# Kernel tuning notes

Measured on AMD Instinct MI355X. Metric: run time of the kernel, lower is better.

## Reference

```python
import jax, jax.numpy as jnp
import numpy as np

D_MODEL, N_HEADS, D_FF = 1024, 16, 4096
B, L, PREFIX = 2, 2048, 512
EPS = 1e-5


def _ln(x, w, b):
    mu = jnp.mean(x, axis=-1, keepdims=True)
    var = jnp.mean((x - mu) ** 2, axis=-1, keepdims=True)
    return (x - mu) * jax.lax.rsqrt(var + EPS) * w + b


def setup_inputs() -> dict:
    key = jax.random.key(0)
    ks = jax.random.split(key, 5)
    d, f = D_MODEL, D_FF
    return {
        "x": jax.random.normal(ks[0], (B, L, d), jnp.float32),
        "ln1_w": jnp.ones((d,), jnp.float32),
        "ln1_b": jnp.zeros((d,), jnp.float32),
        "in_proj_w": jax.random.normal(ks[1], (3 * d, d), jnp.float32) / np.sqrt(d),
        "in_proj_b": jnp.zeros((3 * d,), jnp.float32),
        "out_w": jax.random.normal(ks[2], (d, d), jnp.float32) / np.sqrt(d),
        "out_b": jnp.zeros((d,), jnp.float32),
        "ln2_w": jnp.ones((d,), jnp.float32),
        "ln2_b": jnp.zeros((d,), jnp.float32),
        "fc1_w": jax.random.normal(ks[3], (f, d), jnp.float32) / np.sqrt(d),
        "fc1_b": jnp.zeros((f,), jnp.float32),
        "fc2_w": jax.random.normal(ks[4], (d, f), jnp.float32) / np.sqrt(f),
        "fc2_b": jnp.zeros((d,), jnp.float32),
        "prefix_len": PREFIX,
    }


def reference(x, ln1_w, ln1_b, in_proj_w, in_proj_b, out_w, out_b,
              ln2_w, ln2_b, fc1_w, fc1_b, fc2_w, fc2_b, prefix_len):
    Bv, Lv, d = x.shape
    H = N_HEADS
    hd = d // H
    m = prefix_len

    # additive prefix-decoder mask (L, L): allowed if j < m, or (i >= m and j <= i)
    i = jnp.arange(Lv)[:, None]
    j = jnp.arange(Lv)[None, :]
    allowed = (j < m) | ((i >= m) & (j <= i))
    mask = jnp.where(allowed, 0.0, -jnp.inf).astype(x.dtype)

    h = _ln(x, ln1_w, ln1_b)
    qkv = h @ in_proj_w.T + in_proj_b                      # [B, L, 3d]
    q, k, v = jnp.split(qkv, 3, axis=-1)
    q = q.reshape(Bv, Lv, H, hd)
    k = k.reshape(Bv, Lv, H, hd)
    v = v.reshape(Bv, Lv, H, hd)
    scale = 1.0 / np.sqrt(hd)
    scores = jnp.einsum("bihd,bjhd->bhij", q, k) * scale   # [B, H, L, L]
    attn = jax.nn.softmax(scores + mask, axis=-1)
    ctx = jnp.einsum("bhij,bjhd->bihd", attn, v).reshape(Bv, Lv, d)
    sa = ctx @ out_w.T + out_b
    x = x + sa

    h = _ln(x, ln2_w, ln2_b)
    ff = jax.nn.gelu(h @ fc1_w.T + fc1_b, approximate=False) @ fc2_w.T + fc2_b
    return x + ff
```

## Files before the change

kernel.cpp:

```cpp
#include <hip/hip_runtime.h>
#include <cstdint>
#include <cstddef>

#define DM   1024
#define NH   16
#define HD   64
#define DFF  4096
#define BB   2
#define LL   2048
#define MM   (BB*LL)

using short8 = __attribute__((ext_vector_type(8))) short;
using f32x4  = __attribute__((ext_vector_type(4))) float;

__device__ __forceinline__ unsigned short f2bf(float f) {
  union { float f; uint32_t u; } v; v.f = f;
  uint32_t u = v.u;
  uint32_t r = (u + 0x7fffu + ((u >> 16) & 1u)) >> 16;
  return (unsigned short)r;
}

__device__ __forceinline__ uint32_t cvtpk_bf16(float a, float b) {
  uint32_t r;
  asm("v_cvt_pk_bf16_f32 %0, %1, %2" : "=v"(r) : "v"(a), "v"(b));
  return r;
}

__device__ __forceinline__ float exp2_fast(float x) {
  float r;
  asm("v_exp_f32 %0, %1" : "=v"(r) : "v"(x));
  return r;
}

__device__ __forceinline__ float rcp_fast(float x) {
  float r;
  asm("v_rcp_f32 %0, %1" : "=v"(r) : "v"(x));
  return r;
}

__device__ __forceinline__ float gelu_tanh(float v) {
  float y = v * (0.7978845608028654f + 0.035677408136300125f * v * v);
  float e = exp2_fast(y * 2.885390081777927f);
  float tnh = 1.0f - 2.0f * rcp_fast(1.0f + e);
  return 0.5f * v * (1.0f + tnh);
}

#define GLDS16(gp, lp) \
  __builtin_amdgcn_global_load_lds((const __attribute__((address_space(1))) uint32_t*)(gp), \
                                   (__attribute__((address_space(3))) uint32_t*)(lp), 16, 0, 0)

__device__ __forceinline__ void ln_row_body(const float* __restrict__ x,
                                            const float* __restrict__ w,
                                            const float* __restrict__ b,
                                            unsigned short* __restrict__ out,
                                            int row, int t) {
  float4 v = ((const float4*)(x + (size_t)row * DM))[t];
  float s  = v.x + v.y + v.z + v.w;
  float sq = v.x*v.x + v.y*v.y + v.z*v.z + v.w*v.w;
  #pragma unroll
  for (int o = 32; o; o >>= 1) { s += __shfl_down(s, o); sq += __shfl_down(sq, o); }
  __shared__ float sh[8];
  if ((t & 63) == 0) { sh[t >> 6] = s; sh[4 + (t >> 6)] = sq; }
  __syncthreads();
  float S  = sh[0] + sh[1] + sh[2] + sh[3];
  float SQ = sh[4] + sh[5] + sh[6] + sh[7];
  float mu  = S * (1.0f / DM);
  float var = SQ * (1.0f / DM) - mu * mu;
  float rs  = rsqrtf(var + 1e-5f);
  float4 wv = ((const float4*)w)[t];
  float4 bv = ((const float4*)b)[t];
  ushort4 o;
  o.x = f2bf((v.x - mu) * rs * wv.x + bv.x);
  o.y = f2bf((v.y - mu) * rs * wv.y + bv.y);
  o.z = f2bf((v.z - mu) * rs * wv.z + bv.z);
  o.w = f2bf((v.w - mu) * rs * wv.w + bv.w);
  ((ushort4*)(out + (size_t)row * DM))[t] = o;
}

__global__ __launch_bounds__(256) void convert_f32_bf16(const float* __restrict__ in,
                                                        unsigned short* __restrict__ out, int n4) {
  int i = blockIdx.x * 256 + threadIdx.x;
  if (i < n4) {
    float4 v = ((const float4*)in)[i];
    ushort4 o;
    o.x = f2bf(v.x); o.y = f2bf(v.y); o.z = f2bf(v.z); o.w = f2bf(v.w);
    ((ushort4*)out)[i] = o;
  }
}

__global__ __launch_bounds__(256) void prep_kernel(const float* __restrict__ x,
                                                   const float* __restrict__ ln1_w,
                                                   const float* __restrict__ ln1_b,
                                                   unsigned short* __restrict__ h1,
                                                   const float* __restrict__ s0, unsigned short* __restrict__ d0, int n0,
                                                   const float* __restrict__ s1, unsigned short* __restrict__ d1, int n1,
                                                   const float* __restrict__ s2, unsigned short* __restrict__ d2, int n2,
                                                   const float* __restrict__ s3, unsigned short* __restrict__ d3, int n3) {
  if (blockIdx.x < MM) {
    ln_row_body(x, ln1_w, ln1_b, h1, blockIdx.x, threadIdx.x);
    return;
  }
  const int cb = blockIdx.x - MM;
  const int tid = cb * 256 + threadIdx.x;
  const int stride = (gridDim.x - MM) * 256;
  for (int i = tid; i < n0; i += stride) {
    float4 v = ((const float4*)s0)[i];
    ushort4 o; o.x = f2bf(v.x); o.y = f2bf(v.y); o.z = f2bf(v.z); o.w = f2bf(v.w);
    ((ushort4*)d0)[i] = o;
  }
  for (int i = tid; i < n1; i += stride) {
    float4 v = ((const float4*)s1)[i];
    ushort4 o; o.x = f2bf(v.x); o.y = f2bf(v.y); o.z = f2bf(v.z); o.w = f2bf(v.w);
    ((ushort4*)d1)[i] = o;
  }
  for (int i = tid; i < n2; i += stride) {
    float4 v = ((const float4*)s2)[i];
    ushort4 o; o.x = f2bf(v.x); o.y = f2bf(v.y); o.z = f2bf(v.z); o.w = f2bf(v.w);
    ((ushort4*)d2)[i] = o;
  }
  for (int i = tid; i < n3; i += stride) {
    float4 v = ((const float4*)s3)[i];
    ushort4 o; o.x = f2bf(v.x); o.y = f2bf(v.y); o.z = f2bf(v.z); o.w = f2bf(v.w);
    ((ushort4*)d3)[i] = o;
  }
}

__global__ __launch_bounds__(256) void ln_kernel(const float* __restrict__ x,
                                                 const float* __restrict__ w,
                                                 const float* __restrict__ b,
                                                 unsigned short* __restrict__ out) {
  ln_row_body(x, w, b, out, blockIdx.x, threadIdx.x);
}

template <int EPI, int VT>
__global__ __launch_bounds__(512) void gemm8(const unsigned short* __restrict__ A,
                                             const unsigned short* __restrict__ Bw,
                                             const float* __restrict__ bias,
                                             unsigned short* __restrict__ Cout,
                                             unsigned short* __restrict__ vt,
                                             int M, int N, int K, int lda, int ldb) {
  __shared__ unsigned short As[2][256 * 64];
  __shared__ unsigned short Bs[2][256 * 64];
  const int t = threadIdx.x;
  const int l = t & 63, lr = l & 15, lg = l >> 4;
  const int wid = t >> 6, wm = wid >> 2, wn = wid & 3;

  int bx = blockIdx.x, by = blockIdx.y;
  {
    const int gx = gridDim.x;
    const int total = gx * gridDim.y;
    if ((total & 7) == 0) {
      int lin = by * gx + bx;
      int lin2 = (lin & 7) * (total >> 3) + (lin >> 3);
      bx = lin2 % gx;
      by = lin2 / gx;
    }
  }
  const int m0 = by * 256, n0 = bx * 256;

  f32x4 acc[8][4];
  #pragma unroll
  for (int mi = 0; mi < 8; ++mi)
    #pragma unroll
    for (int ni = 0; ni < 4; ++ni) acc[mi][ni] = {0.f, 0.f, 0.f, 0.f};

  const int rowt = t >> 3, sw = (t & 7) ^ (rowt & 7);
  const unsigned short* Ag = A  + (size_t)(m0 + rowt) * lda + sw * 8;
  const unsigned short* Bg = Bw + (size_t)(n0 + rowt) * ldb + sw * 8;
  const size_t r64A = (size_t)64 * lda;
  const size_t r64B = (size_t)64 * ldb;

  const int rs = lr & 7;
  const int segA = (lg ^ rs) * 8;
  const int segB = ((lg + 4) ^ rs) * 8;

  const int nt = K >> 6;

  auto stage = [&](int kt, int buf) {
    const int k0 = kt << 6;
    char* Ad = (char*)&As[buf][0] + t * 16;
    char* Bd = (char*)&Bs[buf][0] + t * 16;
    #pragma unroll
    for (int g = 0; g < 4; ++g) GLDS16(Ag + k0 + g * r64A, Ad + g * 8192);
    #pragma unroll
    for (int g = 0; g < 4; ++g) GLDS16(Bg + k0 + g * r64B, Bd + g * 8192);
  };

  auto compute = [&](const unsigned short* __restrict__ Ab,
                     const unsigned short* __restrict__ Bb) {
    short8 bfr[4][2];
    #pragma unroll
    for (int ni = 0; ni < 4; ++ni) {
      const int row = wn * 64 + ni * 16 + lr;
      bfr[ni][0] = *(const short8*)&Bb[row * 64 + segA];
      bfr[ni][1] = *(const short8*)&Bb[row * 64 + segB];
    }
    __builtin_amdgcn_s_setprio(1);
    #pragma unroll
    for (int mp = 0; mp < 4; ++mp) {
      short8 af[2][2];
      #pragma unroll
      for (int q = 0; q < 2; ++q) {
        const int row = wm * 128 + (mp * 2 + q) * 16 + lr;
        af[q][0] = *(const short8*)&Ab[row * 64 + segA];
        af[q][1] = *(const short8*)&Ab[row * 64 + segB];
      }
      #pragma unroll
      for (int q = 0; q < 2; ++q)
        #pragma unroll
        for (int ni = 0; ni < 4; ++ni) {
          acc[mp * 2 + q][ni] = __builtin_amdgcn_mfma_f32_16x16x32_bf16(af[q][0], bfr[ni][0], acc[mp * 2 + q][ni], 0, 0, 0);
          acc[mp * 2 + q][ni] = __builtin_amdgcn_mfma_f32_16x16x32_bf16(af[q][1], bfr[ni][1], acc[mp * 2 + q][ni], 0, 0, 0);
        }
    }
    __builtin_amdgcn_s_setprio(0);
  };

  stage(0, 0);
  __syncthreads();

  for (int kt = 0; kt < nt; kt += 2) {
    if (kt + 1 < nt) stage(kt + 1, 1);
    compute(As[0], Bs[0]);
    __syncthreads();
    if (kt + 2 < nt) stage(kt + 2, 0);
    compute(As[1], Bs[1]);
    __syncthreads();
  }

  if (VT && n0 >= 2 * DM) {
    #pragma unroll
    for (int mi = 0; mi < 8; ++mi) {
      int row = m0 + wm * 128 + mi * 16 + lg * 4;
      int b = row >> 11, j = row & (LL - 1);
      #pragma unroll
      for (int ni = 0; ni < 4; ++ni) {
        int col = n0 + wn * 64 + ni * 16 + lr;
        int hd_ = col - 2 * DM;
        float bv = bias[col];
        uint2 pk;
        pk.x = cvtpk_bf16(acc[mi][ni][0] + bv, acc[mi][ni][1] + bv);
        pk.y = cvtpk_bf16(acc[mi][ni][2] + bv, acc[mi][ni][3] + bv);
        *(uint2*)&vt[(size_t)(b * 1024 + hd_) * LL + j] = pk;
      }
    }
    return;
  }

  #pragma unroll
  for (int mi = 0; mi < 8; ++mi) {
    int row = m0 + wm * 128 + mi * 16 + lg * 4;
    #pragma unroll
    for (int ni = 0; ni < 4; ++ni) {
      int col = n0 + wn * 64 + ni * 16 + lr;
      float bv = bias[col];
      #pragma unroll
      for (int r = 0; r < 4; ++r) {
        float v = acc[mi][ni][r] + bv;
        size_t idx = (size_t)(row + r) * N + col;
        if (EPI == 0) {
          Cout[idx] = f2bf(v);
        } else {
          Cout[idx] = f2bf(gelu_tanh(v));
        }
      }
    }
  }
}

template <int EPI, int BM>
__global__ __launch_bounds__(256) void gemm_bt(const unsigned short* __restrict__ A,
                                               const unsigned short* __restrict__ Bw,
                                               const float* __restrict__ bias,
                                               const float* __restrict__ res,
                                               void* __restrict__ Cout,
                                               int M, int N, int K, int lda, int ldb) {
  constexpr int MI   = BM / 32;
  constexpr int ABUF = BM * 64;
  __shared__ unsigned short As[2 * ABUF];
  __shared__ unsigned short Bs[2 * 64 * 64];
  const int t = threadIdx.x;
  const int l = t & 63, lr = l & 15, lg = l >> 4;
  const int w = t >> 6, wm = w >> 1, wn = w & 1;

  int bx = blockIdx.x, by = blockIdx.y;
  {
    const int gx = gridDim.x;
    const int total = gx * gridDim.y;
    if ((total & 7) == 0) {
      int lin = by * gx + bx;
      int lin2 = (lin & 7) * (total >> 3) + (lin >> 3);
      bx = lin2 % gx;
      by = lin2 / gx;
    }
  }
  const int m0 = by * BM, n0 = bx * 64;

  f32x4 acc[MI][2];
  #pragma unroll
  for (int mi = 0; mi < MI; ++mi)
    #pragma unroll
    for (int ni = 0; ni < 2; ++ni) acc[mi][ni] = {0.f, 0.f, 0.f, 0.f};

  const int rowt = t >> 3, sw = (t & 7) ^ (rowt & 7);
  const unsigned short* Ag = A  + (size_t)(m0 + rowt) * lda + sw * 8;
  const unsigned short* Bg = Bw + (size_t)(n0 + rowt) * ldb + sw * 8;
  char* AsB = (char*)As + t * 16;
  char* BsB = (char*)Bs + t * 16;
  const size_t r32A = (size_t)32 * lda;
  const size_t r32B = (size_t)32 * ldb;

  const int rs = lr & 7;
  const int segA = (lg ^ rs) * 8;
  const int segB = ((lg + 4) ^ rs) * 8;

  #pragma unroll
  for (int g = 0; g < MI; ++g) GLDS16(Ag + g * r32A, AsB + g * 4096);
  GLDS16(Bg,        BsB);
  GLDS16(Bg + r32B, BsB + 4096);

  int cur = 0;
  for (int k0 = 0; k0 < K; k0 += 64, cur ^= 1) {
    __syncthreads();
    const int kn = k0 + 64;
    if (kn < K) {
      char* An = AsB + (cur ^ 1) * (ABUF * 2);
      char* Bn = BsB + (cur ^ 1) * 8192;
      #pragma unroll
      for (int g = 0; g < MI; ++g) GLDS16(Ag + kn + g * r32A, An + g * 4096);
      GLDS16(Bg + kn,        Bn);
      GLDS16(Bg + kn + r32B, Bn + 4096);
    }
    const unsigned short* Ab = As + cur * ABUF;
    const unsigned short* Bb = Bs + cur * (64 * 64);
    short8 af[MI][2], bfr[2][2];
    #pragma unroll
    for (int mi = 0; mi < MI; ++mi) {
      const int row = wm * (BM / 2) + mi * 16 + lr;
      af[mi][0] = *(const short8*)&Ab[row * 64 + segA];
      af[mi][1] = *(const short8*)&Ab[row * 64 + segB];
    }
    #pragma unroll
    for (int ni = 0; ni < 2; ++ni) {
      const int row = wn * 32 + ni * 16 + lr;
      bfr[ni][0] = *(const short8*)&Bb[row * 64 + segA];
      bfr[ni][1] = *(const short8*)&Bb[row * 64 + segB];
    }
    #pragma unroll
    for (int mi = 0; mi < MI; ++mi)
      #pragma unroll
      for (int ni = 0; ni < 2; ++ni) {
        acc[mi][ni] = __builtin_amdgcn_mfma_f32_16x16x32_bf16(af[mi][0], bfr[ni][0], acc[mi][ni], 0, 0, 0);
        acc[mi][ni] = __builtin_amdgcn_mfma_f32_16x16x32_bf16(af[mi][1], bfr[ni][1], acc[mi][ni], 0, 0, 0);
      }
  }

  #pragma unroll
  for (int mi = 0; mi < MI; ++mi) {
    int row = m0 + wm * (BM / 2) + mi * 16 + lg * 4;
    #pragma unroll
    for (int ni = 0; ni < 2; ++ni) {
      int col = n0 + wn * 32 + ni * 16 + lr;
      float bv = (EPI == 3) ? 0.f : bias[col];
      #pragma unroll
      for (int r = 0; r < 4; ++r) {
        float v = acc[mi][ni][r] + bv;
        size_t idx = (size_t)(row + r) * N + col;
        if (EPI == 0) {
          ((unsigned short*)Cout)[idx] = f2bf(v);
        } else if (EPI == 1) {
          ((float*)Cout)[idx] = res[idx] + v;
        } else if (EPI == 2) {
          ((unsigned short*)Cout)[idx] = f2bf(gelu_tanh(v));
        } else {
          ((float*)Cout)[idx] += v;
        }
      }
    }
  }
}

__global__ __launch_bounds__(512) void attn_kernel(const unsigned short* __restrict__ qkv,
                                                   const unsigned short* __restrict__ vt,
                                                   const int* __restrict__ prefix,
                                                   unsigned short* __restrict__ ctx) {
  __shared__ unsigned short Ks[2][64 * 64];
  __shared__ unsigned short Vs[2][64 * 64];
  __shared__ unsigned short Plds[8][16][72];
  const int t = threadIdx.x, w = t >> 6, l = t & 63, lr = l & 15, lg = l >> 4;
  const int bh = blockIdx.y, b = bh >> 4, h = bh & 15;
  const int ib = gridDim.x - 1 - blockIdx.x;
  const int i0 = ib * 128, iw = i0 + w * 16;
  const int m = *prefix;
  const float C = 0.125f * 1.44269504088896f;

  const int r0 = t >> 3, s0 = t & 7, swz = s0 ^ (r0 & 7);
  const unsigned short* Kg0 = qkv + (size_t)(b * LL + r0) * 3072 + DM + h * 64 + swz * 8;
  const unsigned short* Vg0 = vt + (size_t)(bh * 64 + r0) * LL + swz * 8;
  char* KdB = (char*)Ks + t * 16;
  char* VdB = (char*)Vs + t * 16;
  const int rs = lr & 7;
  const int segA = (lg ^ rs) * 8;
  const int segB = ((lg + 4) ^ rs) * 8;

  short8 qf[2];
  {
    const unsigned short* qrow = qkv + (size_t)(b * LL + iw + lr) * 3072 + h * 64;
    qf[0] = *(const short8*)(qrow + lg * 8);
    qf[1] = *(const short8*)(qrow + 32 + lg * 8);
  }
  short8 ones;
  #pragma unroll
  for (int e = 0; e < 8; ++e) ones[e] = (short)0x3F80;

  f32x4 Ot[4];
  #pragma unroll
  for (int dt = 0; dt < 4; ++dt) Ot[dt] = {0.f, 0.f, 0.f, 0.f};
  f32x4 Osum = {0.f, 0.f, 0.f, 0.f};

  const int jmax = (i0 + 128 <= m) ? m : (i0 + 128);
  const int nb = (jmax + 63) >> 6;
  const int i_abs = iw + lr;

  GLDS16(Kg0, KdB);
  GLDS16(Vg0, VdB);

  for (int c = 0; c < nb; ++c) {
    __syncthreads();
    if (c + 1 < nb) {
      const size_t jn = (size_t)(c + 1) * 64;
      const int pn = (c + 1) & 1;
      GLDS16(Kg0 + jn * 3072, KdB + pn * 8192);
      GLDS16(Vg0 + jn,        VdB + pn * 8192);
    }
    const int jt = c * 64, p = c & 1;

    f32x4 sc[4];
    #pragma unroll
    for (int nt = 0; nt < 4; ++nt) {
      sc[nt] = {0.f, 0.f, 0.f, 0.f};
      const int row = nt * 16 + lr;
      short8 kf0 = *(const short8*)&Ks[p][row * 64 + segA];
      short8 kf1 = *(const short8*)&Ks[p][row * 64 + segB];
      sc[nt] = __builtin_amdgcn_mfma_f32_16x16x32_bf16(kf0, qf[0], sc[nt], 0, 0, 0);
      sc[nt] = __builtin_amdgcn_mfma_f32_16x16x32_bf16(kf1, qf[1], sc[nt], 0, 0, 0);
    }
    const bool full = (jt + 64 <= m) || (iw >= m && jt + 64 <= iw + 1);
    #pragma unroll
    for (int nt = 0; nt < 4; ++nt) {
      float p0 = exp2_fast(sc[nt][0] * C);
      float p1 = exp2_fast(sc[nt][1] * C);
      float p2 = exp2_fast(sc[nt][2] * C);
      float p3 = exp2_fast(sc[nt][3] * C);
      if (!full) {
        const int jb = jt + nt * 16 + lg * 4;
        const bool causal_i = (i_abs >= m);
        p0 = ((jb + 0 < m) || (causal_i && jb + 0 <= i_abs)) ? p0 : 0.f;
        p1 = ((jb + 1 < m) || (causal_i && jb + 1 <= i_abs)) ? p1 : 0.f;
        p2 = ((jb + 2 < m) || (causal_i && jb + 2 <= i_abs)) ? p2 : 0.f;
        p3 = ((jb + 3 < m) || (causal_i && jb + 3 <= i_abs)) ? p3 : 0.f;
      }
      uint2 pk;
      pk.x = cvtpk_bf16(p0, p1);
      pk.y = cvtpk_bf16(p2, p3);
      *(uint2*)&Plds[w][lr][nt * 16 + lg * 4] = pk;
    }
    short8 paf0 = *(const short8*)&Plds[w][lr][lg * 8];
    short8 paf1 = *(const short8*)&Plds[w][lr][32 + lg * 8];
    #pragma unroll
    for (int dt = 0; dt < 4; ++dt) {
      const int row = dt * 16 + lr;
      short8 vf0 = *(const short8*)&Vs[p][row * 64 + segA];
      short8 vf1 = *(const short8*)&Vs[p][row * 64 + segB];
      Ot[dt] = __builtin_amdgcn_mfma_f32_16x16x32_bf16(paf0, vf0, Ot[dt], 0, 0, 0);
      Ot[dt] = __builtin_amdgcn_mfma_f32_16x16x32_bf16(paf1, vf1, Ot[dt], 0, 0, 0);
    }
    Osum = __builtin_amdgcn_mfma_f32_16x16x32_bf16(paf0, ones, Osum, 0, 0, 0);
    Osum = __builtin_amdgcn_mfma_f32_16x16x32_bf16(paf1, ones, Osum, 0, 0, 0);
  }
  #pragma unroll
  for (int r = 0; r < 4; ++r) {
    float inv = 1.0f / Osum[r];
    size_t row = (size_t)(b * LL + iw + lg * 4 + r);
    #pragma unroll
    for (int dt = 0; dt < 4; ++dt)
      ctx[row * DM + h * 64 + dt * 16 + lr] = f2bf(Ot[dt][r] * inv);
  }
}

extern "C" void kernel_launch(void* const* d_in, const int* in_sizes, int n_in,
                              void* d_out, int out_size, void* d_ws, size_t ws_size,
                              hipStream_t stream) {
  const float* x        = (const float*)d_in[0];
  const float* ln1_w    = (const float*)d_in[1];
  const float* ln1_b    = (const float*)d_in[2];
  const float* in_proj_w= (const float*)d_in[3];
  const float* in_proj_b= (const float*)d_in[4];
  const float* out_w    = (const float*)d_in[5];
  const float* out_b    = (const float*)d_in[6];
  const float* ln2_w    = (const float*)d_in[7];
  const float* ln2_b    = (const float*)d_in[8];
  const float* fc1_w    = (const float*)d_in[9];
  const float* fc1_b    = (const float*)d_in[10];
  const float* fc2_w    = (const float*)d_in[11];
  const float* fc2_b    = (const float*)d_in[12];
  const int*   prefix   = (const int*)d_in[13];
  float* outp = (float*)d_out;

  char* ws = (char*)d_ws;
  unsigned short* slab  = (unsigned short*)ws;
  float*          x2    = (float*)(ws + ((size_t)8 << 20));
  unsigned short* vtb   = (unsigned short*)(ws + ((size_t)8 << 20));
  unsigned short* wslab = (unsigned short*)(ws + ((size_t)24 << 20));
  unsigned short* qkv   = (unsigned short*)(ws + ((size_t)32 << 20));
  unsigned short* wfc2  = (unsigned short*)(ws + ((size_t)32 << 20));
  unsigned short* ffh   = (unsigned short*)(ws + ((size_t)40 << 20));
  const bool big = ws_size >= ((size_t)72 << 20);
  const bool wd  = ws_size >= ((size_t)80 << 20);

  unsigned short* w_in  = (unsigned short*)(ws + ((size_t)24 << 20));
  unsigned short* w_out = (unsigned short*)(ws + ((size_t)30 << 20));
  unsigned short* w_fc1 = (unsigned short*)(ws + ((size_t)64 << 20));
  unsigned short* w_fc2 = (unsigned short*)(ws + ((size_t)72 << 20));
  unsigned short* ffm32 = (unsigned short*)(ws + ((size_t)32 << 20));

  if (wd) {
    prep_kernel<<<MM + 1024, 256, 0, stream>>>(x, ln1_w, ln1_b, slab,
                                               in_proj_w, w_in, 3072 * 1024 / 4,
                                               out_w, w_out, 1024 * 1024 / 4,
                                               fc1_w, w_fc1, 4096 * 1024 / 4,
                                               fc2_w, w_fc2, 1024 * 4096 / 4);
  } else {
    convert_f32_bf16<<<3072, 256, 0, stream>>>(in_proj_w, wslab, 3072 * 1024 / 4);
    ln_kernel<<<MM, 256, 0, stream>>>(x, ln1_w, ln1_b, slab);
  }

  gemm8<0, 1><<<dim3(3072 / 256, MM / 256), 512, 0, stream>>>(slab, wd ? w_in : wslab, in_proj_b, qkv, vtb, MM, 3072, 1024, 1024, 1024);
  attn_kernel<<<dim3(LL / 128, BB * NH), 512, 0, stream>>>(qkv, vtb, prefix, slab);
  if (!wd) convert_f32_bf16<<<1024, 256, 0, stream>>>(out_w, wslab, 1024 * 1024 / 4);
  gemm_bt<1, 64><<<dim3(1024 / 64, MM / 64), 256, 0, stream>>>(slab, wd ? w_out : wslab, out_b, x, x2, MM, 1024, 1024, 1024, 1024);

  ln_kernel<<<MM, 256, 0, stream>>>(x2, ln2_w, ln2_b, slab);
  if (wd) {
    gemm8<2, 0><<<dim3(4096 / 256, MM / 256), 512, 0, stream>>>(slab, w_fc1, fc1_b, ffm32, nullptr, MM, 4096, 1024, 1024, 1024);
    gemm_bt<1, 64><<<dim3(1024 / 64, MM / 64), 256, 0, stream>>>(ffm32, w_fc2, fc2_b, x2, outp, MM, 1024, 4096, 4096, 4096);
  } else {
    convert_f32_bf16<<<4096, 256, 0, stream>>>(fc1_w, wslab, 4096 * 1024 / 4);
    convert_f32_bf16<<<4096, 256, 0, stream>>>(fc2_w, wfc2, 1024 * 4096 / 4);
    if (big) {
      unsigned short* ffmid = (unsigned short*)(ws + ((size_t)40 << 20));
      gemm8<2, 0><<<dim3(4096 / 256, MM / 256), 512, 0, stream>>>(slab, wslab, fc1_b, ffmid, nullptr, MM, 4096, 1024, 1024, 1024);
      gemm_bt<1, 64><<<dim3(1024 / 64, MM / 64), 256, 0, stream>>>(ffmid, wfc2, fc2_b, x2, outp, MM, 1024, 4096, 4096, 4096);
    } else {
      gemm_bt<2, 128><<<dim3(2048 / 64, MM / 128), 256, 0, stream>>>(slab, wslab, fc1_b, nullptr, ffh, MM, 2048, 1024, 1024, 1024);
      gemm_bt<1, 64><<<dim3(1024 / 64, MM / 64), 256, 0, stream>>>(ffh, wfc2, fc2_b, x2, outp, MM, 1024, 2048, 2048, 4096);
      gemm_bt<2, 128><<<dim3(2048 / 64, MM / 128), 256, 0, stream>>>(slab, wslab + (size_t)2048 * 1024, fc1_b + 2048, nullptr, ffh, MM, 2048, 1024, 1024, 1024);
      gemm_bt<3, 64><<<dim3(1024 / 64, MM / 64), 256, 0, stream>>>(ffh, wfc2 + 2048, nullptr, nullptr, outp, MM, 1024, 2048, 2048, 4096);
    }
  }
}
```

Measured before the change: 221.7 us.

## Replace 256x256 GEMM tile kernel with 128x128 tile, 256-thread variant

Swaps the 512-thread 256x256-tile, K=64-step GEMM used for the QKV and FC1 projections for a 256-thread 128x128-tile kernel with K=32 steps and no LDS XOR swizzle. The smaller tiles give more blocks and lower LDS and register use per block, which may improve occupancy and wave balance. In exchange, data reuse per tile drops, barriers per K become more frequent, and unswizzled LDS reads may cause bank conflicts.

```diff
diff --git a/kernel.cpp b/kernel.cpp
--- a/kernel.cpp
+++ b/kernel.cpp
@@ -133,17 +133,17 @@
 }
 
 template <int EPI, int VT>
-__global__ __launch_bounds__(512) void gemm8(const unsigned short* __restrict__ A,
-                                             const unsigned short* __restrict__ Bw,
-                                             const float* __restrict__ bias,
-                                             unsigned short* __restrict__ Cout,
-                                             unsigned short* __restrict__ vt,
-                                             int M, int N, int K, int lda, int ldb) {
-  __shared__ unsigned short As[2][256 * 64];
-  __shared__ unsigned short Bs[2][256 * 64];
+__global__ __launch_bounds__(256) void gemm128(const unsigned short* __restrict__ A,
+                                               const unsigned short* __restrict__ Bw,
+                                               const float* __restrict__ bias,
+                                               unsigned short* __restrict__ Cout,
+                                               unsigned short* __restrict__ vt,
+                                               int M, int N, int K, int lda, int ldb) {
+  __shared__ unsigned short As[2][128 * 32];
+  __shared__ unsigned short Bs[2][128 * 32];
   const int t = threadIdx.x;
   const int l = t & 63, lr = l & 15, lg = l >> 4;
-  const int wid = t >> 6, wm = wid >> 2, wn = wid & 3;
+  const int w = t >> 6, wm = w >> 1, wn = w & 1;
 
   int bx = blockIdx.x, by = blockIdx.y;
   {
@@ -156,82 +156,62 @@
       by = lin2 / gx;
     }
   }
-  const int m0 = by * 256, n0 = bx * 256;
-
-  f32x4 acc[8][4];
-  #pragma unroll
-  for (int mi = 0; mi < 8; ++mi)
+  const int m0 = by * 128, n0 = bx * 128;
+
+  f32x4 acc[4][4];
+  #pragma unroll
+  for (int mi = 0; mi < 4; ++mi)
     #pragma unroll
     for (int ni = 0; ni < 4; ++ni) acc[mi][ni] = {0.f, 0.f, 0.f, 0.f};
 
-  const int rowt = t >> 3, sw = (t & 7) ^ (rowt & 7);
-  const unsigned short* Ag = A  + (size_t)(m0 + rowt) * lda + sw * 8;
-  const unsigned short* Bg = Bw + (size_t)(n0 + rowt) * ldb + sw * 8;
+  const unsigned short* Ag = A  + (size_t)(m0 + (t >> 2)) * lda + (t & 3) * 8;
+  const unsigned short* Bg = Bw + (size_t)(n0 + (t >> 2)) * ldb + (t & 3) * 8;
   const size_t r64A = (size_t)64 * lda;
   const size_t r64B = (size_t)64 * ldb;
 
-  const int rs = lr & 7;
-  const int segA = (lg ^ rs) * 8;
-  const int segB = ((lg + 4) ^ rs) * 8;
-
-  const int nt = K >> 6;
-
-  auto stage = [&](int kt, int buf) {
-    const int k0 = kt << 6;
+  auto stage = [&](int k0, int buf) {
     char* Ad = (char*)&As[buf][0] + t * 16;
     char* Bd = (char*)&Bs[buf][0] + t * 16;
-    #pragma unroll
-    for (int g = 0; g < 4; ++g) GLDS16(Ag + k0 + g * r64A, Ad + g * 8192);
-    #pragma unroll
-    for (int g = 0; g < 4; ++g) GLDS16(Bg + k0 + g * r64B, Bd + g * 8192);
+    GLDS16(Ag + k0,        Ad);
+    GLDS16(Ag + k0 + r64A, Ad + 4096);
+    GLDS16(Bg + k0,        Bd);
+    GLDS16(Bg + k0 + r64B, Bd + 4096);
   };
 
   auto compute = [&](const unsigned short* __restrict__ Ab,
                      const unsigned short* __restrict__ Bb) {
-    short8 bfr[4][2];
-    #pragma unroll
-    for (int ni = 0; ni < 4; ++ni) {
-      const int row = wn * 64 + ni * 16 + lr;
-      bfr[ni][0] = *(const short8*)&Bb[row * 64 + segA];
-      bfr[ni][1] = *(const short8*)&Bb[row * 64 + segB];
-    }
+    short8 af[4], bfr[4];
+    #pragma unroll
+    for (int mi = 0; mi < 4; ++mi)
+      af[mi] = *(const short8*)&Ab[(wm * 64 + mi * 16 + lr) * 32 + lg * 8];
+    #pragma unroll
+    for (int ni = 0; ni < 4; ++ni)
+      bfr[ni] = *(const short8*)&Bb[(wn * 64 + ni * 16 + lr) * 32 + lg * 8];
     __builtin_amdgcn_s_setprio(1);
     #pragma unroll
-    for (int mp = 0; mp < 4; ++mp) {
-      short8 af[2][2];
+    for (int mi = 0; mi < 4; ++mi)
       #pragma unroll
-      for (int q = 0; q < 2; ++q) {
-        const int row = wm * 128 + (mp * 2 + q) * 16 + lr;
-        af[q][0] = *(const short8*)&Ab[row * 64 + segA];
-        af[q][1] = *(const short8*)&Ab[row * 64 + segB];
-      }
-      #pragma unroll
-      for (int q = 0; q < 2; ++q)
-        #pragma unroll
-        for (int ni = 0; ni < 4; ++ni) {
-          acc[mp * 2 + q][ni] = __builtin_amdgcn_mfma_f32_16x16x32_bf16(af[q][0], bfr[ni][0], acc[mp * 2 + q][ni], 0, 0, 0);
-          acc[mp * 2 + q][ni] = __builtin_amdgcn_mfma_f32_16x16x32_bf16(af[q][1], bfr[ni][1], acc[mp * 2 + q][ni], 0, 0, 0);
-        }
-    }
+      for (int ni = 0; ni < 4; ++ni)
+        acc[mi][ni] = __builtin_amdgcn_mfma_f32_16x16x32_bf16(af[mi], bfr[ni], acc[mi][ni], 0, 0, 0);
     __builtin_amdgcn_s_setprio(0);
   };
 
   stage(0, 0);
   __syncthreads();
 
-  for (int kt = 0; kt < nt; kt += 2) {
-    if (kt + 1 < nt) stage(kt + 1, 1);
+  for (int k0 = 0; k0 < K; k0 += 64) {
+    if (k0 + 32 < K) stage(k0 + 32, 1);
     compute(As[0], Bs[0]);
     __syncthreads();
-    if (kt + 2 < nt) stage(kt + 2, 0);
+    if (k0 + 64 < K) stage(k0 + 64, 0);
     compute(As[1], Bs[1]);
     __syncthreads();
   }
 
   if (VT && n0 >= 2 * DM) {
     #pragma unroll
-    for (int mi = 0; mi < 8; ++mi) {
-      int row = m0 + wm * 128 + mi * 16 + lg * 4;
+    for (int mi = 0; mi < 4; ++mi) {
+      int row = m0 + wm * 64 + mi * 16 + lg * 4;
       int b = row >> 11, j = row & (LL - 1);
       #pragma unroll
       for (int ni = 0; ni < 4; ++ni) {
@@ -248,8 +228,8 @@
   }
 
   #pragma unroll
-  for (int mi = 0; mi < 8; ++mi) {
-    int row = m0 + wm * 128 + mi * 16 + lg * 4;
+  for (int mi = 0; mi < 4; ++mi) {
+    int row = m0 + wm * 64 + mi * 16 + lg * 4;
     #pragma unroll
     for (int ni = 0; ni < 4; ++ni) {
       int col = n0 + wn * 64 + ni * 16 + lr;
@@ -535,21 +515,21 @@
     ln_kernel<<<MM, 256, 0, stream>>>(x, ln1_w, ln1_b, slab);
   }
 
-  gemm8<0, 1><<<dim3(3072 / 256, MM / 256), 512, 0, stream>>>(slab, wd ? w_in : wslab, in_proj_b, qkv, vtb, MM, 3072, 1024, 1024, 1024);
+  gemm128<0, 1><<<dim3(3072 / 128, MM / 128), 256, 0, stream>>>(slab, wd ? w_in : wslab, in_proj_b, qkv, vtb, MM, 3072, 1024, 1024, 1024);
   attn_kernel<<<dim3(LL / 128, BB * NH), 512, 0, stream>>>(qkv, vtb, prefix, slab);
   if (!wd) convert_f32_bf16<<<1024, 256, 0, stream>>>(out_w, wslab, 1024 * 1024 / 4);
   gemm_bt<1, 64><<<dim3(1024 / 64, MM / 64), 256, 0, stream>>>(slab, wd ? w_out : wslab, out_b, x, x2, MM, 1024, 1024, 1024, 1024);
 
   ln_kernel<<<MM, 256, 0, stream>>>(x2, ln2_w, ln2_b, slab);
   if (wd) {
-    gemm8<2, 0><<<dim3(4096 / 256, MM / 256), 512, 0, stream>>>(slab, w_fc1, fc1_b, ffm32, nullptr, MM, 4096, 1024, 1024, 1024);
+    gemm128<2, 0><<<dim3(4096 / 128, MM / 128), 256, 0, stream>>>(slab, w_fc1, fc1_b, ffm32, nullptr, MM, 4096, 1024, 1024, 1024);
     gemm_bt<1, 64><<<dim3(1024 / 64, MM / 64), 256, 0, stream>>>(ffm32, w_fc2, fc2_b, x2, outp, MM, 1024, 4096, 4096, 4096);
   } else {
     convert_f32_bf16<<<4096, 256, 0, stream>>>(fc1_w, wslab, 4096 * 1024 / 4);
     convert_f32_bf16<<<4096, 256, 0, stream>>>(fc2_w, wfc2, 1024 * 4096 / 4);
     if (big) {
       unsigned short* ffmid = (unsigned short*)(ws + ((size_t)40 << 20));
-      gemm8<2, 0><<<dim3(4096 / 256, MM / 256), 512, 0, stream>>>(slab, wslab, fc1_b, ffmid, nullptr, MM, 4096, 1024, 1024, 1024);
+      gemm128<2, 0><<<dim3(4096 / 128, MM / 128), 256, 0, stream>>>(slab, wslab, fc1_b, ffmid, nullptr, MM, 4096, 1024, 1024, 1024);
       gemm_bt<1, 64><<<dim3(1024 / 64, MM / 64), 256, 0, stream>>>(ffmid, wfc2, fc2_b, x2, outp, MM, 1024, 4096, 4096, 4096);
     } else {
       gemm_bt<2, 128><<<dim3(2048 / 64, MM / 128), 256, 0, stream>>>(slab, wslab, fc1_b, nullptr, ffh, MM, 2048, 1024, 1024, 1024);
```

New measurement: 243.3 us. 1.1x slower.
